# Kernel optimization log

Measured on AMD Instinct MI355X. Metric: run time of the kernel, lower is better.

Reference implementation:

```python
import jax, jax.numpy as jnp
import numpy as np

B, S, D, H = 4, 2048, 1024, 16
DK = D // H
THETA = 10000.0

def _trunc_normal(key, shape, in_f, out_f):
    std = (2.0 / (in_f + out_f)) ** 0.5
    return jax.random.truncated_normal(key, -3.0, 3.0, shape, jnp.float32) * std

def setup_inputs() -> dict:
    key = jax.random.key(0)
    kx, kq, kk, kv, ko = jax.random.split(key, 5)
    x = jax.random.normal(kx, (B, S, D), jnp.float32)
    wq = _trunc_normal(kq, (D, D), D, D)
    wk = _trunc_normal(kk, (D, D), D, D)
    wv = _trunc_normal(kv, (D, D), D, D)
    wo = _trunc_normal(ko, (D, D), D, D)
    token_positions = jnp.arange(S, dtype=jnp.int32)
    return {"x": x, "wq": wq, "wk": wk, "wv": wv, "wo": wo,
            "token_positions": token_positions}

def _rope_tables(token_positions, d_k, theta):
    # freq_cos/sin with each frequency duplicated pairwise: (d j) layout
    exponent = jnp.arange(0, d_k, 2, dtype=jnp.float32) / d_k
    freq = 1.0 / (theta ** exponent)            # [d_k/2]
    f = token_positions.astype(jnp.float32)[:, None] * freq[None, :]  # [s, d_k/2]
    cos = jnp.repeat(jnp.cos(f), 2, axis=-1)    # [s, d_k]
    sin = jnp.repeat(jnp.sin(f), 2, axis=-1)
    return cos, sin

def _rotate_half(x):
    x_even = x[..., 0::2]
    x_odd = x[..., 1::2]
    return jnp.stack((-x_odd, x_even), axis=-1).reshape(x.shape)

def reference(x, wq, wk, wv, wo, token_positions):
    b, s, d = x.shape
    # projections: y = x @ W^T  (weight stored [out, in])
    def proj(w):
        y = jnp.einsum('bsi,oi->bso', x, w)
        return y.reshape(b, s, H, DK).transpose(0, 2, 1, 3)  # [b,h,s,dk]
    q, k, v = proj(wq), proj(wk), proj(wv)
    cos, sin = _rope_tables(token_positions, DK, THETA)      # [s,dk]
    q = q * cos + _rotate_half(q) * sin
    k = k * cos + _rotate_half(k) * sin
    scores = jnp.einsum('bhnd,bhmd->bhnm', q, k) / jnp.sqrt(jnp.float32(DK))
    mask = jnp.tril(jnp.ones((s, s), dtype=bool))
    scores = jnp.where(mask, scores, -jnp.inf)
    attn = jax.nn.softmax(scores, axis=-1)
    out = jnp.einsum('bhnm,bhmd->bhnd', attn, v)
    out = out.transpose(0, 2, 1, 3).reshape(b, s, d)
    return jnp.einsum('bsi,oi->bso', out, wo)
```

## Files before the change

### kernel.cpp

```cpp
#include <hip/hip_runtime.h>
#include <hip/hip_bf16.h>
#include <stdint.h>
#include <math.h>

static constexpr int kS  = 2048;
static constexpr int kH  = 16;
static constexpr int kDK = 64;
static constexpr int kD  = 1024;
static constexpr int kB  = 4;
static constexpr int kM  = kB * kS;

typedef __bf16 bf16;
typedef __attribute__((ext_vector_type(8))) __bf16 bf16x8;
typedef __attribute__((ext_vector_type(4))) __bf16 bf16x4;
typedef __attribute__((ext_vector_type(4))) float f32x4;

__device__ __forceinline__ void gload_lds16(const bf16* g, bf16* l) {
  __builtin_amdgcn_global_load_lds((__attribute__((address_space(1))) void*)(void*)g,
                                   (__attribute__((address_space(3))) void*)l, 16, 0, 0);
}

__global__ void cvt_f32_bf16(const float* __restrict__ in, bf16* __restrict__ out, int n4) {
  int i = blockIdx.x * blockDim.x + threadIdx.x;
  if (i >= n4) return;
  float4 v = reinterpret_cast<const float4*>(in)[i];
  bf16x4 o;
  o[0] = (bf16)v.x; o[1] = (bf16)v.y; o[2] = (bf16)v.z; o[3] = (bf16)v.w;
  reinterpret_cast<bf16x4*>(out)[i] = o;
}

__global__ void cvt_w4(const float* __restrict__ w0, const float* __restrict__ w1,
                       const float* __restrict__ w2, const float* __restrict__ w3,
                       bf16* __restrict__ o0, bf16* __restrict__ o1,
                       bf16* __restrict__ o2, bf16* __restrict__ o3, int n4) {
  int i = blockIdx.x * blockDim.x + threadIdx.x;
  if (i >= n4) return;
  const int sel = blockIdx.y;
  const float* in = (sel == 0) ? w0 : (sel == 1) ? w1 : (sel == 2) ? w2 : w3;
  bf16* out      = (sel == 0) ? o0 : (sel == 1) ? o1 : (sel == 2) ? o2 : o3;
  float4 v = reinterpret_cast<const float4*>(in)[i];
  bf16x4 o;
  o[0] = (bf16)v.x; o[1] = (bf16)v.y; o[2] = (bf16)v.z; o[3] = (bf16)v.w;
  reinterpret_cast<bf16x4*>(out)[i] = o;
}

template<int BM>
__device__ __forceinline__ void gemm_body(const bf16* __restrict__ A,
                                          const bf16* __restrict__ W,
                                          void* __restrict__ dst,
                                          int K, int mode, int brow, int bcol) {
  constexpr int MF  = BM / 32;
  constexpr int ACH = BM / 64;

  __shared__ __align__(16) bf16 As[2][2][BM * 32];
  __shared__ __align__(16) bf16 Bs[2][2][128 * 32];

  const int tid = threadIdx.x;
  const int l   = tid & 63;
  const int w   = tid >> 6;
  const int wr = (w >> 1) * (BM / 2);
  const int wc = (w & 1) * 64;

  f32x4 acc[MF][4] = {};

  const int lrow = l >> 2;
  const int lcol = (l & 3) * 8;
  const int fr  = l & 15;
  const int fk  = (l >> 4) * 8;

  const int nk = K >> 6;

  auto STAGE = [&](int buf, int kt) {
#pragma unroll
    for (int h = 0; h < 2; ++h) {
      const int k0 = (kt << 6) + h * 32;
#pragma unroll
      for (int c2 = 0; c2 < ACH; ++c2) {
        const int c = w * ACH + c2;
        gload_lds16(A + (size_t)(brow + c * 16 + lrow) * K + k0 + lcol, &As[buf][h][c * 512]);
      }
#pragma unroll
      for (int c2 = 0; c2 < 2; ++c2) {
        const int c = w * 2 + c2;
        gload_lds16(W + (size_t)(bcol + c * 16 + lrow) * K + k0 + lcol, &Bs[buf][h][c * 512]);
      }
    }
  };

  STAGE(0, 0);
  __syncthreads();

  int cur = 0;
  for (int kt = 0; kt < nk; ++kt) {
    if (kt + 1 < nk) STAGE(cur ^ 1, kt + 1);

#pragma unroll
    for (int h = 0; h < 2; ++h) {
      bf16x8 af[MF], bfm[4];
#pragma unroll
      for (int m = 0; m < MF; ++m) af[m]  = *(const bf16x8*)&As[cur][h][(wr + m * 16 + fr) * 32 + fk];
#pragma unroll
      for (int n = 0; n < 4; ++n)  bfm[n] = *(const bf16x8*)&Bs[cur][h][(wc + n * 16 + fr) * 32 + fk];
#pragma unroll
      for (int m = 0; m < MF; ++m)
#pragma unroll
        for (int n = 0; n < 4; ++n)
          acc[m][n] = __builtin_amdgcn_mfma_f32_16x16x32_bf16(af[m], bfm[n], acc[m][n], 0, 0, 0);
    }

    __syncthreads();
    cur ^= 1;
  }

  const int frow = (l >> 4) * 4;
  if (mode == 0) {
    bf16* out = (bf16*)dst;
#pragma unroll
    for (int m = 0; m < MF; ++m) {
#pragma unroll
      for (int n = 0; n < 4; ++n) {
        const int col = bcol + wc + n * 16 + fr;
        const int h = col >> 6, dk = col & 63;
#pragma unroll
        for (int r = 0; r < 4; ++r) {
          const int row = brow + wr + m * 16 + frow + r;
          const int b = row >> 11, s = row & (kS - 1);
          out[((((size_t)b * kH + h) * kS + s) << 6) + dk] = (bf16)acc[m][n][r];
        }
      }
    }
  } else {
    float* out = (float*)dst;
#pragma unroll
    for (int m = 0; m < MF; ++m) {
#pragma unroll
      for (int n = 0; n < 4; ++n) {
        const int col = bcol + wc + n * 16 + fr;
#pragma unroll
        for (int r = 0; r < 4; ++r) {
          const int row = brow + wr + m * 16 + frow + r;
          out[(size_t)row * kD + col] = acc[m][n][r];
        }
      }
    }
  }
}

template<int BM>
__global__ __launch_bounds__(256) void gemm_k(const bf16* __restrict__ A,
                                              const bf16* __restrict__ W,
                                              void* __restrict__ dst, int K, int mode) {
  gemm_body<BM>(A, W, dst, K, mode, blockIdx.x * BM, blockIdx.y * 128);
}

__global__ __launch_bounds__(256) void gemm_qkv(const bf16* __restrict__ A,
                                                const bf16* __restrict__ wq,
                                                const bf16* __restrict__ wk,
                                                const bf16* __restrict__ wv,
                                                bf16* __restrict__ Qb,
                                                bf16* __restrict__ Kb,
                                                bf16* __restrict__ Vb, int K) {
  const int by = blockIdx.y;
  const int sel = by >> 3;
  const bf16* W = (sel == 0) ? wq : (sel == 1) ? wk : wv;
  bf16* dst     = (sel == 0) ? Qb : (sel == 1) ? Kb : Vb;
  gemm_body<128>(A, W, dst, K, 0, blockIdx.x * 128, (by & 7) * 128);
}

__global__ void rope_kernel(bf16* __restrict__ Q, bf16* __restrict__ Kb,
                            const int* __restrict__ pos, int np) {
  int idx = blockIdx.x * blockDim.x + threadIdx.x;
  if (idx >= 2 * np) return;
  const bool isQ = (idx < np);
  bf16* T = isQ ? Q : Kb;
  int id = isQ ? idx : idx - np;
  const int i = id & 31;
  const int s = (id >> 5) & (kS - 1);
  const float p = (float)pos[s];
  const float freq = __expf(-0.2878231366242557f * (float)i);
  const float f = p * freq;
  float sn, cs;
  sincosf(f, &sn, &cs);
  const float sc = isQ ? (0.125f * 1.4426950408889634f) : 1.0f;
  const size_t off = (size_t)id * 2;
  const float e = (float)T[off], o = (float)T[off + 1];
  T[off]     = (bf16)((e * cs - o * sn) * sc);
  T[off + 1] = (bf16)((o * cs + e * sn) * sc);
}

__global__ __launch_bounds__(256) void attn_fwd(const bf16* __restrict__ Q,
                                                const bf16* __restrict__ Kb,
                                                const bf16* __restrict__ Vb,
                                                bf16* __restrict__ O) {
  const int bh = blockIdx.x;
  const int qt = (int)gridDim.y - 1 - (int)blockIdx.y;
  const int tid = threadIdx.x;
  const int l = tid & 63;
  const int w = tid >> 6;

  __shared__ __align__(16) bf16 Ks[64 * 64];
  __shared__ __align__(16) bf16 Vt[64 * 64];
  __shared__ __align__(16) bf16 Pl[4][16 * 64];

  const int q0 = qt * 64 + w * 16;
  const int fr  = l & 15;
  const int fkg = l >> 4;
  const int fkg4 = fkg << 2;
  const size_t base = (size_t)bh * kS * kDK;

  bf16x8 aq[2];
#pragma unroll
  for (int kc = 0; kc < 2; ++kc)
    aq[kc] = *(const bf16x8*)&Q[base + (size_t)(q0 + fr) * kDK + kc * 32 + fkg * 8];

  f32x4 ao[4] = {};
  float m_r = -1e30f, l_r = 0.f;

  const int nt = qt + 1;

  const int krow = tid >> 3;
  const int kcol = (tid & 7) * 8;
  const int dk0  = w * 16;

  bf16x8 kreg0, kreg1, vreg0, vreg1;
  {
    const size_t kb0 = base + (size_t)krow * kDK + kcol;
    kreg0 = *(const bf16x8*)&Kb[kb0];
    kreg1 = *(const bf16x8*)&Kb[kb0 + 32 * kDK];
    const size_t vb0 = base + (size_t)l * kDK + dk0;
    vreg0 = *(const bf16x8*)&Vb[vb0];
    vreg1 = *(const bf16x8*)&Vb[vb0 + 8];
  }

  for (int j = 0; j < nt; ++j) {
    {
      const int r0 = krow, r1 = krow + 32;
      *(bf16x8*)&Ks[r0 * 64 + (kcol ^ ((r0 & 7) << 3))] = kreg0;
      *(bf16x8*)&Ks[r1 * 64 + (kcol ^ ((r1 & 7) << 3))] = kreg1;
#pragma unroll
      for (int e = 0; e < 8; ++e) {
        const int d0 = dk0 + e, d1 = dk0 + 8 + e;
        Vt[d0 * 64 + (l ^ ((d0 & 7) << 3))] = vreg0[e];
        Vt[d1 * 64 + (l ^ ((d1 & 7) << 3))] = vreg1[e];
      }
    }
    __syncthreads();

    if (j + 1 < nt) {
      const size_t kb0 = base + (size_t)((j + 1) * 64 + krow) * kDK + kcol;
      kreg0 = *(const bf16x8*)&Kb[kb0];
      kreg1 = *(const bf16x8*)&Kb[kb0 + 32 * kDK];
      const size_t vb0 = base + (size_t)((j + 1) * 64 + l) * kDK + dk0;
      vreg0 = *(const bf16x8*)&Vb[vb0];
      vreg1 = *(const bf16x8*)&Vb[vb0 + 8];
    }

    const bool diag = (j == nt - 1);

    f32x4 sc[4] = {};
#pragma unroll
    for (int nf = 0; nf < 4; ++nf) {
      if (!diag || nf <= w) {
#pragma unroll
        for (int kc = 0; kc < 2; ++kc) {
          const int row = nf * 16 + fr;
          bf16x8 bk = *(const bf16x8*)&Ks[row * 64 + ((kc * 32 + fkg * 8) ^ ((row & 7) << 3))];
          sc[nf] = __builtin_amdgcn_mfma_f32_16x16x32_bf16(bk, aq[kc], sc[nf], 0, 0, 0);
        }
      }
    }

    const int qloc = w * 16 + fr;
    float p[4][4];
    float mx = -INFINITY;
#pragma unroll
    for (int nf = 0; nf < 4; ++nf)
#pragma unroll
      for (int r = 0; r < 4; ++r) {
        float s = sc[nf][r];
        if (diag && (nf * 16 + fkg4 + r) > qloc) s = -INFINITY;
        p[nf][r] = s;
        mx = fmaxf(mx, s);
      }
    mx = fmaxf(mx, __shfl_xor(mx, 16));
    mx = fmaxf(mx, __shfl_xor(mx, 32));

    if (__any(mx > m_r + 11.5f)) {
      const float mnew = fmaxf(m_r, mx);
      const float sf = __builtin_amdgcn_exp2f(m_r - mnew);
      l_r *= sf;
      m_r = mnew;
#pragma unroll
      for (int r = 0; r < 4; ++r) {
        const float sfq = __shfl(sf, (l & 48) + fkg4 + r);
#pragma unroll
        for (int n = 0; n < 4; ++n) ao[n][r] *= sfq;
      }
    }

    float rs = 0.f;
#pragma unroll
    for (int nf = 0; nf < 4; ++nf)
#pragma unroll
      for (int r = 0; r < 4; ++r) {
        p[nf][r] = __builtin_amdgcn_exp2f(p[nf][r] - m_r);
        rs += p[nf][r];
      }
    rs += __shfl_xor(rs, 16);
    rs += __shfl_xor(rs, 32);
    l_r += rs;

#pragma unroll
    for (int nf = 0; nf < 4; ++nf) {
      bf16x4 p4;
#pragma unroll
      for (int r = 0; r < 4; ++r) p4[r] = (bf16)p[nf][r];
      *(bf16x4*)&Pl[w][fr * 64 + ((nf * 16 + fkg4) ^ ((fr & 7) << 3))] = p4;
    }
    bf16x8 pa[2];
#pragma unroll
    for (int kc2 = 0; kc2 < 2; ++kc2)
      pa[kc2] = *(const bf16x8*)&Pl[w][fr * 64 + ((kc2 * 32 + fkg * 8) ^ ((fr & 7) << 3))];

#pragma unroll
    for (int kc2 = 0; kc2 < 2; ++kc2) {
      if (kc2 == 0 || !diag || w >= 2) {
#pragma unroll
        for (int n = 0; n < 4; ++n) {
          const int row = n * 16 + fr;
          bf16x8 bv = *(const bf16x8*)&Vt[row * 64 + ((kc2 * 32 + fkg * 8) ^ ((row & 7) << 3))];
          ao[n] = __builtin_amdgcn_mfma_f32_16x16x32_bf16(pa[kc2], bv, ao[n], 0, 0, 0);
        }
      }
    }
    __syncthreads();
  }

  const int b = bh >> 4, h = bh & 15;
  float lq[4];
#pragma unroll
  for (int r = 0; r < 4; ++r) lq[r] = __shfl(l_r, (l & 48) + fkg4 + r);
#pragma unroll
  for (int n = 0; n < 4; ++n)
#pragma unroll
    for (int r = 0; r < 4; ++r) {
      const int qg = q0 + fkg4 + r;
      const float ov = ao[n][r] / lq[r];
      O[((size_t)(b * kS + qg) << 10) + h * 64 + n * 16 + fr] = (bf16)ov;
    }
}

extern "C" void kernel_launch(void* const* d_in, const int* in_sizes, int n_in,
                              void* d_out, int out_size, void* d_ws, size_t ws_size,
                              hipStream_t stream) {
  const float* x  = (const float*)d_in[0];
  const float* wq = (const float*)d_in[1];
  const float* wk = (const float*)d_in[2];
  const float* wv = (const float*)d_in[3];
  const float* wo = (const float*)d_in[4];
  const int* pos  = (const int*)d_in[5];

  bf16* xb  = (bf16*)d_ws;
  bf16* wqb = xb  + (size_t)kM * kD;
  bf16* wkb = wqb + (size_t)kD * kD;
  bf16* wvb = wkb + (size_t)kD * kD;
  bf16* wob = wvb + (size_t)kD * kD;
  bf16* Qb  = wob + (size_t)kD * kD;
  bf16* Kbf = Qb  + (size_t)64 * kS * kDK;
  bf16* Vbf = Kbf + (size_t)64 * kS * kDK;
  bf16* Ob  = Vbf + (size_t)64 * kS * kDK;

  {
    int n4 = kM * kD / 4;
    cvt_f32_bf16<<<(n4 + 255) / 256, 256, 0, stream>>>(x, xb, n4);
    n4 = kD * kD / 4;
    cvt_w4<<<dim3((n4 + 255) / 256, 4), 256, 0, stream>>>(wq, wk, wv, wo, wqb, wkb, wvb, wob, n4);
  }

  gemm_qkv<<<dim3(kM / 128, 24), 256, 0, stream>>>(xb, wqb, wkb, wvb, Qb, Kbf, Vbf, kD);

  const int np = 64 * kS * 32;
  rope_kernel<<<(2 * np) / 256, 256, 0, stream>>>(Qb, Kbf, pos, np);

  dim3 ga(64, kS / 64);
  attn_fwd<<<ga, 256, 0, stream>>>(Qb, Kbf, Vbf, Ob);

  gemm_k<128><<<dim3(kM / 128, kD / 128), 256, 0, stream>>>(Ob, wob, d_out, kD, 1);
}
```

Before: 278.6 us.

## Triple-buffer GEMM K-tiles with vmcnt waits and use hardware sin/cos in RoPE

The projection GEMM moves from a double-buffered 64-wide K step with two __syncthreads per iteration to a three-stage ring of 32-wide K tiles. It waits on outstanding global-to-LDS loads with explicit s_waitcnt vmcnt and one barrier per iteration, which keeps two tiles in flight to hide load latency. The RoPE kernel replaces sincosf with range-reduced hardware v_sin/v_cos builtins, trading a little accuracy for fewer instructions. The hand-set vmcnt(4) count depends on how many loads each stage issues, so the synchronisation is fragile if the tile configuration changes.

```diff
diff --git a/kernel.cpp b/kernel.cpp
--- a/kernel.cpp
+++ b/kernel.cpp
@@ -52,8 +52,8 @@
   constexpr int MF  = BM / 32;
   constexpr int ACH = BM / 64;
 
-  __shared__ __align__(16) bf16 As[2][2][BM * 32];
-  __shared__ __align__(16) bf16 Bs[2][2][128 * 32];
+  __shared__ __align__(16) bf16 As[3][BM * 32];
+  __shared__ __align__(16) bf16 Bs[3][128 * 32];
 
   const int tid = threadIdx.x;
   const int l   = tid & 63;
@@ -68,48 +68,49 @@
   const int fr  = l & 15;
   const int fk  = (l >> 4) * 8;
 
-  const int nk = K >> 6;
+  const int nk = K >> 5;
 
   auto STAGE = [&](int buf, int kt) {
-#pragma unroll
-    for (int h = 0; h < 2; ++h) {
-      const int k0 = (kt << 6) + h * 32;
-#pragma unroll
-      for (int c2 = 0; c2 < ACH; ++c2) {
-        const int c = w * ACH + c2;
-        gload_lds16(A + (size_t)(brow + c * 16 + lrow) * K + k0 + lcol, &As[buf][h][c * 512]);
-      }
-#pragma unroll
-      for (int c2 = 0; c2 < 2; ++c2) {
-        const int c = w * 2 + c2;
-        gload_lds16(W + (size_t)(bcol + c * 16 + lrow) * K + k0 + lcol, &Bs[buf][h][c * 512]);
-      }
+    const int k0 = kt << 5;
+#pragma unroll
+    for (int c2 = 0; c2 < ACH; ++c2) {
+      const int c = w * ACH + c2;
+      gload_lds16(A + (size_t)(brow + c * 16 + lrow) * K + k0 + lcol, &As[buf][c * 512]);
+    }
+#pragma unroll
+    for (int c2 = 0; c2 < 2; ++c2) {
+      const int c = w * 2 + c2;
+      gload_lds16(W + (size_t)(bcol + c * 16 + lrow) * K + k0 + lcol, &Bs[buf][c * 512]);
     }
   };
 
   STAGE(0, 0);
-  __syncthreads();
+  STAGE(1, 1);
 
   int cur = 0;
   for (int kt = 0; kt < nk; ++kt) {
-    if (kt + 1 < nk) STAGE(cur ^ 1, kt + 1);
-
-#pragma unroll
-    for (int h = 0; h < 2; ++h) {
-      bf16x8 af[MF], bfm[4];
-#pragma unroll
-      for (int m = 0; m < MF; ++m) af[m]  = *(const bf16x8*)&As[cur][h][(wr + m * 16 + fr) * 32 + fk];
-#pragma unroll
-      for (int n = 0; n < 4; ++n)  bfm[n] = *(const bf16x8*)&Bs[cur][h][(wc + n * 16 + fr) * 32 + fk];
-#pragma unroll
-      for (int m = 0; m < MF; ++m)
-#pragma unroll
-        for (int n = 0; n < 4; ++n)
-          acc[m][n] = __builtin_amdgcn_mfma_f32_16x16x32_bf16(af[m], bfm[n], acc[m][n], 0, 0, 0);
-    }
-
-    __syncthreads();
-    cur ^= 1;
+    if (kt + 1 < nk) { asm volatile("s_waitcnt vmcnt(4)" ::: "memory"); }
+    else             { asm volatile("s_waitcnt vmcnt(0)" ::: "memory"); }
+    __builtin_amdgcn_s_barrier();
+    __builtin_amdgcn_sched_barrier(0);
+
+    if (kt + 2 < nk) {
+      int s2 = cur + 2; if (s2 >= 3) s2 -= 3;
+      STAGE(s2, kt + 2);
+    }
+
+    bf16x8 af[MF], bfm[4];
+#pragma unroll
+    for (int m = 0; m < MF; ++m) af[m]  = *(const bf16x8*)&As[cur][(wr + m * 16 + fr) * 32 + fk];
+#pragma unroll
+    for (int n = 0; n < 4; ++n)  bfm[n] = *(const bf16x8*)&Bs[cur][(wc + n * 16 + fr) * 32 + fk];
+#pragma unroll
+    for (int m = 0; m < MF; ++m)
+#pragma unroll
+      for (int n = 0; n < 4; ++n)
+        acc[m][n] = __builtin_amdgcn_mfma_f32_16x16x32_bf16(af[m], bfm[n], acc[m][n], 0, 0, 0);
+
+    cur = (cur + 1 == 3) ? 0 : cur + 1;
   }
 
   const int frow = (l >> 4) * 4;
@@ -178,9 +179,10 @@
   const int s = (id >> 5) & (kS - 1);
   const float p = (float)pos[s];
   const float freq = __expf(-0.2878231366242557f * (float)i);
-  const float f = p * freq;
-  float sn, cs;
-  sincosf(f, &sn, &cs);
+  const float frev = p * freq * 0.15915494309189535f;
+  const float r = frev - floorf(frev);
+  const float sn = __builtin_amdgcn_sinf(r);
+  const float cs = __builtin_amdgcn_cosf(r);
   const float sc = isQ ? (0.125f * 1.4426950408889634f) : 1.0f;
   const size_t off = (size_t)id * 2;
   const float e = (float)T[off], o = (float)T[off + 1];
```

Measured after the change: 278.0 us. Within noise of the previous version (-0.2%).
